# Kernel optimization log

Measured on AMD Instinct MI355X. Metric: run time of the kernel, lower is better.

Reference implementation:

```python
import jax, jax.numpy as jnp
import numpy as np

N, E, G = 100000, 600000, 64  # nodes, edges, graphs
F_IN, W, EPS = 32, 128, 1e-5


def setup_inputs() -> dict:
    key = jax.random.key(0)
    ks = jax.random.split(key, 16)
    p = lambda k, shape: jax.random.normal(k, shape, dtype=jnp.float32) * 0.1
    z = lambda n: jnp.zeros((n,), jnp.float32)
    o = lambda n: jnp.ones((n,), jnp.float32)
    return {
        "x": jax.random.normal(ks[0], (N, F_IN), dtype=jnp.float32),
        "edge_index": jax.random.randint(ks[1], (2, E), 0, N, dtype=jnp.int32),
        "batch": jnp.sort(jax.random.randint(ks[2], (N,), 0, G, dtype=jnp.int32)),
        # GCNConv layers
        "W1": p(ks[3], (F_IN, W)), "b1": z(W),
        "W2": p(ks[4], (W, W)), "b2": z(W),
        # mlp_first: Linear -> BN -> ReLU -> Linear
        "W3": p(ks[5], (W, W)), "b3": z(W), "g1": o(W), "be1": z(W),
        "W4": p(ks[6], (W, W)), "b4": z(W),
        # mlp: Linear -> BN -> ReLU -> Linear
        "W5": p(ks[7], (W, W // 2)), "b5": z(W // 2), "g2": o(W // 2), "be2": z(W // 2),
        "W6": p(ks[8], (W // 2, 1)), "b6": z(1),
    }


def gcn_conv(x, src, dst, Wt, b):
    # PyG GCNConv with add_self_loops=True: D^-1/2 (A+I) D^-1/2 (x W) + b
    h = x @ Wt  # [N, width]
    deg = jax.ops.segment_sum(jnp.ones(src.shape[0], x.dtype), dst, num_segments=N) + 1.0
    dinv = jax.lax.rsqrt(deg)
    norm = dinv[src] * dinv[dst]  # per-edge normalization
    agg = jax.ops.segment_sum(h[src] * norm[:, None], dst, num_segments=N)
    # self-loop term: norm for (i,i) is 1/deg[i]
    return agg + h * (dinv * dinv)[:, None] + b


def batch_norm(x, g, b):
    # training-mode BatchNorm1d (batch stats, biased var)
    mu = x.mean(axis=0)
    var = jnp.mean((x - mu) ** 2, axis=0)
    return (x - mu) * jax.lax.rsqrt(var + EPS) * g + b


def reference(x, edge_index, batch, W1, b1, W2, b2, W3, b3, g1, be1, W4, b4, W5, b5, g2, be2, W6, b6):
    src, dst = edge_index[0], edge_index[1]
    x = jax.nn.relu(gcn_conv(x, src, dst, W1, b1))
    x = jax.nn.relu(gcn_conv(x, src, dst, W2, b2))
    # mlp_first + ReLU
    x = jax.nn.relu(batch_norm(x @ W3 + b3, g1, be1)) @ W4 + b4
    x = jax.nn.relu(x)
    # global max pool over nodes per graph
    x = jax.ops.segment_max(x, batch, num_segments=G)  # [G, width]
    # final mlp
    x = jax.nn.relu(batch_norm(x @ W5 + b5, g2, be2)) @ W6 + b6
    return x[:, 0]
```

## Files before the change

kernel.cpp:

```cpp
#include <hip/hip_runtime.h>

#define N_NODES 100000
#define N_EDGES 600000
#define N_GRAPHS 64
#define EPS 1e-5f
#define SCAN_BLOCKS 391

typedef unsigned short u16;
typedef unsigned int u32;
typedef __attribute__((ext_vector_type(8))) short bf16x8;
typedef __attribute__((ext_vector_type(4))) float f32x4;

__device__ __forceinline__ float bf2f(u16 u) { return __uint_as_float(((u32)u) << 16); }
__device__ __forceinline__ u16 f2bf(float f) {
    u32 u = __float_as_uint(f);
    u += 0x7FFFu + ((u >> 16) & 1u);
    return (u16)(u >> 16);
}
__device__ __forceinline__ float2 bfx2(u32 v) {
    float2 r;
    r.x = __uint_as_float(v << 16);
    r.y = __uint_as_float(v & 0xFFFF0000u);
    return r;
}

#define WS_COUNTS   ((size_t)0)
#define WS_CURSOR   ((size_t)400384)
#define WS_POOLED   ((size_t)800768)
#define WS_BNSUM    ((size_t)833536)
#define WS_BNSUMSQ  ((size_t)834048)
#define WS_FLAG     ((size_t)834560)
#define ZERO_BYTES  ((size_t)835072)
#define WS_OFFSETS  ((size_t)835072)
#define WS_DINV     ((size_t)1235456)
#define WS_DINV2    ((size_t)1635840)
#define WS_SRCS     ((size_t)2036224)
#define WS_ZF       ((size_t)4436736)
#define WS_CANONW   ((size_t)4453120)
#define WS_BUFA     ((size_t)4578560)
#define WS_BUFB     ((size_t)30178560)

#define CW_W1 0
#define CW_B1 4096
#define CW_W2 4224
#define CW_B2 20608
#define CW_W3 20736
#define CW_B3 37120
#define CW_G1 37248
#define CW_BE1 37376
#define CW_W4 37504
#define CW_B4 53888
#define CW_W5 54016
#define CW_B5 62208
#define CW_G2 62272
#define CW_BE2 62336
#define CW_W6 62400
#define CW_B6 62464

__global__ void detect_kernel(const u32* __restrict__ xraw, int* __restrict__ flag) {
    __shared__ int cnt;
    if (threadIdx.x == 0) cnt = 0;
    __syncthreads();
    int c = 0;
    for (int i = threadIdx.x; i < 2048; i += 256) {
        u32 w = xraw[i];
        float a = fabsf(__uint_as_float((w & 0xFFFFu) << 16));
        if (a == 0.f || (a > 1e-8f && a < 1e4f)) c++;
    }
    atomicAdd(&cnt, c);
    __syncthreads();
    if (threadIdx.x == 0) *flag = (cnt > 1024) ? 1 : 0;
}

__global__ void convx_kernel(const void* __restrict__ xsrc, u16* __restrict__ dst,
                             const int* __restrict__ flag, const float* __restrict__ dinv) {
    int i = blockIdx.x * 256 + threadIdx.x;
    if (i < N_NODES * 32) {
        int r = i >> 5, c = i & 31;
        float v = (*flag) ? bf2f(((const u16*)xsrc)[i]) : ((const float*)xsrc)[i];
        dst[(size_t)(c >> 3) * (N_NODES * 8) + (size_t)r * 8 + (c & 7)] = f2bf(v * dinv[r]);
    }
}

struct SmallArgs {
    const void* src[16];
    int n[16];
    int off[16];
    int cols[16];
};
__global__ void convs_kernel(SmallArgs a, u16* __restrict__ dst, const int* __restrict__ flag) {
    int i = blockIdx.x * 256 + threadIdx.x;
    int isbf = *flag;
#pragma unroll
    for (int j = 0; j < 16; j++)
        if (i < a.n[j]) {
            u16 v = isbf ? ((const u16*)a.src[j])[i] : f2bf(((const float*)a.src[j])[i]);
            if (a.cols[j] > 0) {
                int k = i / a.cols[j];
                int n = i - k * a.cols[j];
                int Kd = a.n[j] / a.cols[j];
                dst[a.off[j] + n * Kd + k] = v;
            } else {
                dst[a.off[j] + i] = v;
            }
        }
}

__global__ void deg_kernel(const int* __restrict__ dst, int* __restrict__ counts) {
    int e = blockIdx.x * 256 + threadIdx.x;
    if (e < N_EDGES) atomicAdd(&counts[dst[e]], 1);
}

__global__ __launch_bounds__(256) void reduce_kernel(const int* __restrict__ counts,
                                                     int* __restrict__ partials) {
    int i = blockIdx.x * 256 + threadIdx.x;
    int v = (i < N_NODES) ? counts[i] : 0;
    for (int off = 32; off > 0; off >>= 1) v += __shfl_down(v, off, 64);
    __shared__ int wsum[4];
    if ((threadIdx.x & 63) == 0) wsum[threadIdx.x >> 6] = v;
    __syncthreads();
    if (threadIdx.x == 0) partials[blockIdx.x] = wsum[0] + wsum[1] + wsum[2] + wsum[3];
}

__global__ __launch_bounds__(512) void scanpart_kernel(int* __restrict__ partials) {
    __shared__ int sc[512];
    int t = threadIdx.x;
    int v = (t < SCAN_BLOCKS) ? partials[t] : 0;
    sc[t] = v;
    __syncthreads();
    for (int off = 1; off < 512; off <<= 1) {
        int u = (t >= off) ? sc[t - off] : 0;
        __syncthreads();
        sc[t] += u;
        __syncthreads();
    }
    if (t < SCAN_BLOCKS) partials[t] = sc[t] - v;
}

__global__ __launch_bounds__(256) void offsets_kernel(const int* __restrict__ counts,
                                                      const int* __restrict__ partials,
                                                      int* __restrict__ offs,
                                                      float* __restrict__ dinv) {
    int i = blockIdx.x * 256 + threadIdx.x;
    int lane = threadIdx.x & 63, wv = threadIdx.x >> 6;
    int v = (i < N_NODES) ? counts[i] : 0;
    int sv = v;
    for (int off = 1; off < 64; off <<= 1) {
        int u = __shfl_up(sv, off, 64);
        if (lane >= off) sv += u;
    }
    __shared__ int wsum[4];
    if (lane == 63) wsum[wv] = sv;
    __syncthreads();
    int wpre = 0;
    for (int w = 0; w < wv; w++) wpre += wsum[w];
    int excl = sv - v + wpre + partials[blockIdx.x];
    if (i < N_NODES) {
        offs[i] = excl;
        dinv[i] = rsqrtf((float)(v + 1));
    }
    if (i == N_NODES - 1) offs[N_NODES] = excl + v;
}

__global__ void scatter_kernel(const int* __restrict__ src, const int* __restrict__ dst,
                               const int* __restrict__ offs, int* __restrict__ cursor,
                               int* __restrict__ srcs) {
    int e = blockIdx.x * 256 + threadIdx.x;
    if (e < N_EDGES) {
        int d = dst[e];
        int p = offs[d] + atomicAdd(&cursor[d], 1);
        srcs[p] = src[e];
    }
}

__global__ __launch_bounds__(256, 8) void agg1_kernel(const u16* __restrict__ xs4,
                                                      const int* __restrict__ offs,
                                                      const int* __restrict__ srcs,
                                                      const float* __restrict__ dinv,
                                                      u16* __restrict__ axs) {
    const int p = blockIdx.x & 3;
    const int r = (blockIdx.x >> 2) * 256 + threadIdx.x;
    if (r >= N_NODES) return;
    const u16* base = xs4 + (size_t)p * (N_NODES * 8);
    float acc[8];
    {
        uint4 own = *(const uint4*)(base + (size_t)r * 8);
        u32 w4[4] = {own.x, own.y, own.z, own.w};
#pragma unroll
        for (int t = 0; t < 4; t++) {
            float2 f = bfx2(w4[t]);
            acc[2 * t] = f.x;
            acc[2 * t + 1] = f.y;
        }
    }
    const int e0 = offs[r], e1 = offs[r + 1];
    for (int e = e0; e < e1; e++) {
        int s = srcs[e];
        uint4 raw = *(const uint4*)(base + (size_t)s * 8);
        u32 w4[4] = {raw.x, raw.y, raw.z, raw.w};
#pragma unroll
        for (int t = 0; t < 4; t++) {
            float2 f = bfx2(w4[t]);
            acc[2 * t] += f.x;
            acc[2 * t + 1] += f.y;
        }
    }
    const float di = dinv[r];
    uint4 outv;
    u32* pk = (u32*)&outv;
#pragma unroll
    for (int t = 0; t < 4; t++)
        pk[t] = (u32)f2bf(acc[2 * t] * di) | ((u32)f2bf(acc[2 * t + 1] * di) << 16);
    *(uint4*)(axs + (size_t)r * 32 + p * 8) = outv;
}

__global__ __launch_bounds__(256, 8) void agg2_kernel(const u16* __restrict__ P2,
                                                      const int* __restrict__ offs,
                                                      const int* __restrict__ srcs,
                                                      const float* __restrict__ dinv,
                                                      const u16* __restrict__ b2,
                                                      u16* __restrict__ x2) {
    const int p = blockIdx.x & 7;
    const int t = threadIdx.x;
    const int r = (blockIdx.x >> 3) * 128 + (t >> 1);
    const int half = t & 1;
    if (r >= N_NODES) return;
    const u16* base = P2 + (size_t)p * (N_NODES * 16) + half * 8;
    float acc[8];
    {
        uint4 own = *(const uint4*)(base + (size_t)r * 16);
        u32 w4[4] = {own.x, own.y, own.z, own.w};
#pragma unroll
        for (int j = 0; j < 4; j++) {
            float2 f = bfx2(w4[j]);
            acc[2 * j] = f.x;
            acc[2 * j + 1] = f.y;
        }
    }
    const int e0 = offs[r], e1 = offs[r + 1];
    for (int e = e0; e < e1; e++) {
        int s = srcs[e];
        uint4 raw = *(const uint4*)(base + (size_t)s * 16);
        u32 w4[4] = {raw.x, raw.y, raw.z, raw.w};
#pragma unroll
        for (int j = 0; j < 4; j++) {
            float2 f = bfx2(w4[j]);
            acc[2 * j] += f.x;
            acc[2 * j + 1] += f.y;
        }
    }
    const float di = dinv[r];
    uint4 bb = *(const uint4*)(b2 + p * 16 + half * 8);
    u32 bw[4] = {bb.x, bb.y, bb.z, bb.w};
    uint4 outv;
    u32* pk = (u32*)&outv;
#pragma unroll
    for (int j = 0; j < 4; j++) {
        float2 fb = bfx2(bw[j]);
        float vx = fmaxf(fmaf(acc[2 * j], di, fb.x), 0.f);
        float vy = fmaxf(fmaf(acc[2 * j + 1], di, fb.y), 0.f);
        pk[j] = (u32)f2bf(vx) | ((u32)f2bf(vy) << 16);
    }
    *(uint4*)(x2 + (size_t)r * 128 + p * 16 + half * 8) = outv;
}

__global__ __launch_bounds__(256, 3) void gemmx_kernel(
    const u16* __restrict__ axs, const u16* __restrict__ W1t, const u16* __restrict__ b1,
    const u16* __restrict__ W2t, u16* __restrict__ P2, const float* __restrict__ dinv, int M) {
    __shared__ __align__(16) u16 ldsA[128 * 40];
    __shared__ __align__(16) u16 ldsB[128 * 136];

    const int tid = threadIdx.x;
    const int wave = tid >> 6;
    const int lane = tid & 63;
    const int l15 = lane & 15;
    const int quad = lane >> 4;
    const int row0 = blockIdx.x * 128 + wave * 32;

    {
        const u32* g = (const u32*)W1t;
        u32* l = (u32*)ldsA;
        for (int i = tid; i < 128 * 16; i += 256) {
            int n = i >> 4, j = i & 15;
            l[n * 20 + j] = g[i];
        }
    }
    {
        const u32* g = (const u32*)W2t;
        u32* l = (u32*)ldsB;
        for (int i = tid; i < 128 * 64; i += 256) {
            int n = i >> 6, j = i & 63;
            l[n * 68 + j] = g[i];
        }
    }

    uint4 gr1[2];
#pragma unroll
    for (int rt = 0; rt < 2; rt++) {
        int r = min(row0 + rt * 16 + l15, M - 1);
        gr1[rt] = *(const uint4*)(axs + (size_t)r * 32 + quad * 8);
    }
    __syncthreads();

    f32x4 acc1[2][8];
#pragma unroll
    for (int rt = 0; rt < 2; rt++)
#pragma unroll
        for (int nt = 0; nt < 8; nt++) acc1[rt][nt] = {0.f, 0.f, 0.f, 0.f};
#pragma unroll
    for (int nt = 0; nt < 8; nt++) {
        bf16x8 bf = *(const bf16x8*)&ldsA[(nt * 16 + l15) * 40 + quad * 8];
        acc1[0][nt] = __builtin_amdgcn_mfma_f32_16x16x32_bf16(
            __builtin_bit_cast(bf16x8, gr1[0]), bf, acc1[0][nt], 0, 0, 0);
        acc1[1][nt] = __builtin_amdgcn_mfma_f32_16x16x32_bf16(
            __builtin_bit_cast(bf16x8, gr1[1]), bf, acc1[1][nt], 0, 0, 0);
    }
    __syncthreads();

    float bcol[8];
#pragma unroll
    for (int nt = 0; nt < 8; nt++) bcol[nt] = bf2f(b1[nt * 16 + l15]);
    u16* tb = ldsA + wave * 1280;
    uint4 gr2[2][4];
#pragma unroll
    for (int kt = 0; kt < 4; kt++) {
#pragma unroll
        for (int rt = 0; rt < 2; rt++)
#pragma unroll
            for (int c2 = 0; c2 < 2; c2++) {
                int nt = 2 * kt + c2;
#pragma unroll
                for (int i = 0; i < 4; i++) {
                    float v = fmaxf(acc1[rt][nt][i] + bcol[nt], 0.f);
                    tb[(rt * 16 + quad * 4 + i) * 40 + c2 * 16 + l15] = f2bf(v);
                }
            }
#pragma unroll
        for (int rt = 0; rt < 2; rt++)
            gr2[rt][kt] = *(const uint4*)&tb[(rt * 16 + l15) * 40 + quad * 8];
    }

    f32x4 acc2[2][8];
#pragma unroll
    for (int rt = 0; rt < 2; rt++)
#pragma unroll
        for (int nt = 0; nt < 8; nt++) acc2[rt][nt] = {0.f, 0.f, 0.f, 0.f};
#pragma unroll
    for (int kt = 0; kt < 4; kt++) {
#pragma unroll
        for (int nt = 0; nt < 8; nt++) {
            bf16x8 bf = *(const bf16x8*)&ldsB[(nt * 16 + l15) * 136 + kt * 32 + quad * 8];
            acc2[0][nt] = __builtin_amdgcn_mfma_f32_16x16x32_bf16(
                __builtin_bit_cast(bf16x8, gr2[0][kt]), bf, acc2[0][nt], 0, 0, 0);
            acc2[1][nt] = __builtin_amdgcn_mfma_f32_16x16x32_bf16(
                __builtin_bit_cast(bf16x8, gr2[1][kt]), bf, acc2[1][nt], 0, 0, 0);
        }
    }

#pragma unroll
    for (int rt = 0; rt < 2; rt++)
#pragma unroll
        for (int i = 0; i < 4; i++) {
            int r = row0 + rt * 16 + quad * 4 + i;
            if (r < M) {
                float ds = dinv[r];
#pragma unroll
                for (int nt = 0; nt < 8; nt++)
                    P2[(size_t)nt * (N_NODES * 16) + (size_t)r * 16 + l15] =
                        f2bf(acc2[rt][nt][i] * ds);
            }
        }
}

__global__ __launch_bounds__(256, 3) void gemm3_kernel(
    const u16* __restrict__ A, const u16* __restrict__ Wt, const u16* __restrict__ bias,
    u16* __restrict__ C, float* __restrict__ bn_sum, float* __restrict__ bn_sumsq, int M) {
    constexpr int KP = 136;
    __shared__ __align__(16) u16 Wl[128 * KP];
    __shared__ float csum[128], csumsq[128];

    const int tid = threadIdx.x;
    const int wave = tid >> 6;
    const int lane = tid & 63;
    const int l15 = lane & 15;
    const int quad = lane >> 4;
    const int row0 = blockIdx.x * 128 + wave * 32;

    uint4 ra[2][4];
    int nd[2];
#pragma unroll
    for (int rt = 0; rt < 2; rt++) {
        nd[rt] = row0 + rt * 16 + l15;
        int r = min(nd[rt], M - 1);
        const u16* ap = A + (size_t)r * 128 + quad * 8;
#pragma unroll
        for (int kt = 0; kt < 4; kt++) ra[rt][kt] = *(const uint4*)(ap + kt * 32);
    }

    {
        const u32* g = (const u32*)Wt;
        u32* l = (u32*)Wl;
        for (int i = tid; i < 128 * 64; i += 256) {
            int n = i >> 6, j = i & 63;
            l[n * 68 + j] = g[i];
        }
    }
    if (tid < 128) {
        csum[tid] = 0.f;
        csumsq[tid] = 0.f;
    }
    __syncthreads();

    f32x4 acc[2][8];
#pragma unroll
    for (int rt = 0; rt < 2; rt++)
#pragma unroll
        for (int nt = 0; nt < 8; nt++) acc[rt][nt] = {0.f, 0.f, 0.f, 0.f};

#pragma unroll
    for (int kt = 0; kt < 4; kt++) {
        bf16x8 a0 = __builtin_bit_cast(bf16x8, ra[0][kt]);
        bf16x8 a1 = __builtin_bit_cast(bf16x8, ra[1][kt]);
#pragma unroll
        for (int nt = 0; nt < 8; nt++) {
            bf16x8 wf = *(const bf16x8*)&Wl[(nt * 16 + l15) * KP + kt * 32 + quad * 8];
            acc[0][nt] = __builtin_amdgcn_mfma_f32_16x16x32_bf16(wf, a0, acc[0][nt], 0, 0, 0);
            acc[1][nt] = __builtin_amdgcn_mfma_f32_16x16x32_bf16(wf, a1, acc[1][nt], 0, 0, 0);
        }
    }

    const bool ok0 = nd[0] < M, ok1 = nd[1] < M;
#pragma unroll
    for (int nt = 0; nt < 8; nt++) {
        uint2 braw = *(const uint2*)(bias + nt * 16 + quad * 4);
        float2 f0 = bfx2(braw.x), f1 = bfx2(braw.y);
        float bb[4] = {f0.x, f0.y, f1.x, f1.y};
        float v0[4], v1[4];
#pragma unroll
        for (int i = 0; i < 4; i++) {
            v0[i] = ok0 ? (acc[0][nt][i] + bb[i]) : 0.f;
            v1[i] = ok1 ? (acc[1][nt][i] + bb[i]) : 0.f;
        }
        if (ok0) {
            uint2 st;
            st.x = (u32)f2bf(v0[0]) | ((u32)f2bf(v0[1]) << 16);
            st.y = (u32)f2bf(v0[2]) | ((u32)f2bf(v0[3]) << 16);
            *(uint2*)(C + (size_t)nd[0] * 128 + nt * 16 + quad * 4) = st;
        }
        if (ok1) {
            uint2 st;
            st.x = (u32)f2bf(v1[0]) | ((u32)f2bf(v1[1]) << 16);
            st.y = (u32)f2bf(v1[2]) | ((u32)f2bf(v1[3]) << 16);
            *(uint2*)(C + (size_t)nd[1] * 128 + nt * 16 + quad * 4) = st;
        }
#pragma unroll
        for (int i = 0; i < 4; i++) {
            float s = v0[i] + v1[i];
            float q = v0[i] * v0[i] + v1[i] * v1[i];
#pragma unroll
            for (int m = 1; m < 16; m <<= 1) {
                s += __shfl_xor(s, m);
                q += __shfl_xor(q, m);
            }
            if (l15 == 0) {
                atomicAdd(&csum[nt * 16 + quad * 4 + i], s);
                atomicAdd(&csumsq[nt * 16 + quad * 4 + i], q);
            }
        }
    }
    __syncthreads();
    if (tid < 128) {
        atomicAdd(&bn_sum[tid], csum[tid]);
        atomicAdd(&bn_sumsq[tid], csumsq[tid]);
    }
}

__global__ __launch_bounds__(256, 3) void gemm4_kernel(
    const u16* __restrict__ A, const u16* __restrict__ Wt, const u16* __restrict__ bias,
    const float* __restrict__ scl, const float* __restrict__ shf,
    const int* __restrict__ batch, u32* __restrict__ pooled, int M) {
    constexpr int KP = 136;
    __shared__ __align__(16) u16 Wl[128 * KP];
    __shared__ u32 lmax[4 * 128];

    const int tid = threadIdx.x;
    const int wave = tid >> 6;
    const int lane = tid & 63;
    const int l15 = lane & 15;
    const int quad = lane >> 4;
    const int row0 = blockIdx.x * 128 + wave * 32;

    uint4 ra[2][4];
#pragma unroll
    for (int rt = 0; rt < 2; rt++) {
        int r = min(row0 + rt * 16 + l15, M - 1);
        const u16* ap = A + (size_t)r * 128 + quad * 8;
#pragma unroll
        for (int kt = 0; kt < 4; kt++) ra[rt][kt] = *(const uint4*)(ap + kt * 32);
    }

    {
        const u32* g = (const u32*)Wt;
        u32* l = (u32*)Wl;
        for (int i = tid; i < 128 * 64; i += 256) {
            int n = i >> 6, j = i & 63;
            l[n * 68 + j] = g[i];
        }
    }
    for (int i = tid; i < 512; i += 256) lmax[i] = 0u;

    const int base = blockIdx.x * 128;
    const int gfirst = batch[min(base, M - 1)];
    const int glast = batch[min(base + 127, M - 1)];
    const bool fast = (glast - gfirst) < 4;
    __syncthreads();

    f32x4 acc[2][8];
#pragma unroll
    for (int rt = 0; rt < 2; rt++)
#pragma unroll
        for (int nt = 0; nt < 8; nt++) acc[rt][nt] = {0.f, 0.f, 0.f, 0.f};

#pragma unroll
    for (int kt = 0; kt < 4; kt++) {
        float s8[8], h8[8];
#pragma unroll
        for (int t = 0; t < 8; t++) {
            s8[t] = scl[kt * 32 + quad * 8 + t];
            h8[t] = shf[kt * 32 + quad * 8 + t];
        }
        bf16x8 af[2];
#pragma unroll
        for (int rt = 0; rt < 2; rt++) {
            u32 w4[4] = {ra[rt][kt].x, ra[rt][kt].y, ra[rt][kt].z, ra[rt][kt].w};
            bf16x8 tmp;
#pragma unroll
            for (int t = 0; t < 4; t++) {
                float2 f = bfx2(w4[t]);
                f.x = fmaxf(fmaf(f.x, s8[2 * t], h8[2 * t]), 0.f);
                f.y = fmaxf(fmaf(f.y, s8[2 * t + 1], h8[2 * t + 1]), 0.f);
                tmp[2 * t] = (short)f2bf(f.x);
                tmp[2 * t + 1] = (short)f2bf(f.y);
            }
            af[rt] = tmp;
        }
#pragma unroll
        for (int nt = 0; nt < 8; nt++) {
            bf16x8 bf = *(const bf16x8*)&Wl[(nt * 16 + l15) * KP + kt * 32 + quad * 8];
            acc[0][nt] = __builtin_amdgcn_mfma_f32_16x16x32_bf16(af[0], bf, acc[0][nt], 0, 0, 0);
            acc[1][nt] = __builtin_amdgcn_mfma_f32_16x16x32_bf16(af[1], bf, acc[1][nt], 0, 0, 0);
        }
    }

    float b[8];
#pragma unroll
    for (int nt = 0; nt < 8; nt++) b[nt] = bf2f(bias[nt * 16 + l15]);
    float cur[8];
#pragma unroll
    for (int nt = 0; nt < 8; nt++) cur[nt] = 0.f;
    int curg = -1;
#pragma unroll
    for (int rt = 0; rt < 2; rt++)
#pragma unroll
        for (int i = 0; i < 4; i++) {
            int r = row0 + rt * 16 + quad * 4 + i;
            if (r < M) {
                int g = batch[r];
                if (g != curg) {
                    if (curg >= 0) {
#pragma unroll
                        for (int nt = 0; nt < 8; nt++)
                            if (cur[nt] > 0.f) {
                                u32 bits = __float_as_uint(cur[nt]);
                                if (fast)
                                    atomicMax(&lmax[(curg - gfirst) * 128 + nt * 16 + l15], bits);
                                else
                                    atomicMax(&pooled[curg * 128 + nt * 16 + l15], bits);
                            }
                    }
                    curg = g;
#pragma unroll
                    for (int nt = 0; nt < 8; nt++) cur[nt] = 0.f;
                }
#pragma unroll
                for (int nt = 0; nt < 8; nt++)
                    cur[nt] = fmaxf(cur[nt], fmaxf(acc[rt][nt][i] + b[nt], 0.f));
            }
        }
    if (curg >= 0) {
#pragma unroll
        for (int nt = 0; nt < 8; nt++)
            if (cur[nt] > 0.f) {
                u32 bits = __float_as_uint(cur[nt]);
                if (fast)
                    atomicMax(&lmax[(curg - gfirst) * 128 + nt * 16 + l15], bits);
                else
                    atomicMax(&pooled[curg * 128 + nt * 16 + l15], bits);
            }
    }
    __syncthreads();
    if (fast) {
        int ngr = glast - gfirst + 1;
        for (int i = tid; i < ngr * 128; i += 256) {
            u32 v = lmax[i];
            if (v) atomicMax(&pooled[gfirst * 128 + i], v);
        }
    }
}

__global__ void bnstats_kernel(float* __restrict__ bn_sum, float* __restrict__ bn_sumsq,
                               const u16* __restrict__ g1, const u16* __restrict__ be1) {
    int c = threadIdx.x;
    if (c < 128) {
        float mu = bn_sum[c] / (float)N_NODES;
        float var = bn_sumsq[c] / (float)N_NODES - mu * mu;
        float rstd = rsqrtf(var + EPS);
        float sc = rstd * bf2f(g1[c]);
        bn_sum[c] = sc;
        bn_sumsq[c] = bf2f(be1[c]) - mu * sc;
    }
}

__global__ __launch_bounds__(256) void head1_kernel(const u32* __restrict__ pooled,
                                                    const u16* __restrict__ W5,
                                                    const u16* __restrict__ b5,
                                                    float* __restrict__ zf) {
    __shared__ float red[4][64];
    int g = blockIdx.x;
    int c = threadIdx.x & 63;
    int kq = threadIdx.x >> 6;
    const u32* prow = pooled + g * 128;
    float p = 0.f;
    for (int k = kq * 32; k < kq * 32 + 32; k++)
        p = fmaf(__uint_as_float(prow[k]), bf2f(W5[k * 64 + c]), p);
    red[kq][c] = p;
    __syncthreads();
    if (kq == 0) zf[g * 64 + c] = red[0][c] + red[1][c] + red[2][c] + red[3][c] + bf2f(b5[c]);
}

__global__ __launch_bounds__(64) void head2_kernel(const float* __restrict__ zf,
                                                   const u16* __restrict__ g2,
                                                   const u16* __restrict__ be2,
                                                   const u16* __restrict__ W6,
                                                   const u16* __restrict__ b6,
                                                   void* __restrict__ outv,
                                                   const int* __restrict__ flag) {
    __shared__ float Z[64][65];
    __shared__ float sc[64], sh[64], w6[64];
    int t = threadIdx.x;
    for (int idx = t; idx < 4096; idx += 64) Z[idx >> 6][idx & 63] = zf[idx];
    w6[t] = bf2f(W6[t]);
    __syncthreads();
    {
        float s = 0.f, sq = 0.f;
        for (int g = 0; g < 64; g++) {
            float v = Z[g][t];
            s += v;
            sq += v * v;
        }
        float mu = s * (1.f / 64.f);
        float var = sq * (1.f / 64.f) - mu * mu;
        float rstd = rsqrtf(var + EPS);
        float scale = rstd * bf2f(g2[t]);
        sc[t] = scale;
        sh[t] = bf2f(be2[t]) - mu * scale;
    }
    __syncthreads();
    float o = 0.f;
    for (int c = 0; c < 64; c++)
        o = fmaf(fmaxf(fmaf(Z[t][c], sc[c], sh[c]), 0.f), w6[c], o);
    float res = o + bf2f(b6[0]);
    if (*flag)
        ((u16*)outv)[t] = f2bf(res);
    else
        ((float*)outv)[t] = res;
}

extern "C" void kernel_launch(void* const* d_in, const int* in_sizes, int n_in, void* d_out,
                              int out_size, void* d_ws, size_t ws_size, hipStream_t stream) {
    const void* x = d_in[0];
    const int* ei = (const int*)d_in[1];
    const int* bat = (const int*)d_in[2];

    char* ws = (char*)d_ws;
    int* counts = (int*)(ws + WS_COUNTS);
    int* cursor = (int*)(ws + WS_CURSOR);
    u32* pooled = (u32*)(ws + WS_POOLED);
    float* bnsum = (float*)(ws + WS_BNSUM);
    float* bnssq = (float*)(ws + WS_BNSUMSQ);
    int* flag = (int*)(ws + WS_FLAG);
    int* offs = (int*)(ws + WS_OFFSETS);
    float* dinv = (float*)(ws + WS_DINV);
    int* partials = (int*)(ws + WS_DINV2);
    int* srcs = (int*)(ws + WS_SRCS);
    float* zf = (float*)(ws + WS_ZF);
    u16* cw = (u16*)(ws + WS_CANONW);
    u16* P2 = (u16*)(ws + WS_BUFA);
    u16* xs4 = (u16*)(ws + WS_BUFB);
    u16* axs = (u16*)(ws + WS_BUFB) + 3200000;
    u16* x2 = (u16*)(ws + WS_BUFB);

    const int* esrc = ei;
    const int* edst = ei + N_EDGES;

    hipMemsetAsync(ws, 0, ZERO_BYTES, stream);
    detect_kernel<<<1, 256, 0, stream>>>((const u32*)x, flag);

    SmallArgs sa;
    const int cw_off[16] = {CW_W1, CW_B1, CW_W2, CW_B2, CW_W3, CW_B3, CW_G1, CW_BE1,
                            CW_W4, CW_B4, CW_W5, CW_B5, CW_G2, CW_BE2, CW_W6, CW_B6};
    const int cw_n[16] = {4096, 128, 16384, 128, 16384, 128, 128, 128,
                          16384, 128, 8192, 64, 64, 64, 64, 1};
    const int cw_c[16] = {128, 0, 128, 0, 128, 0, 0, 0, 128, 0, 0, 0, 0, 0, 0, 0};
    for (int j = 0; j < 16; j++) {
        sa.src[j] = d_in[3 + j];
        sa.n[j] = cw_n[j];
        sa.off[j] = cw_off[j];
        sa.cols[j] = cw_c[j];
    }
    convs_kernel<<<64, 256, 0, stream>>>(sa, cw, flag);

    deg_kernel<<<(N_EDGES + 255) / 256, 256, 0, stream>>>(edst, counts);
    reduce_kernel<<<SCAN_BLOCKS, 256, 0, stream>>>(counts, partials);
    scanpart_kernel<<<1, 512, 0, stream>>>(partials);
    offsets_kernel<<<SCAN_BLOCKS, 256, 0, stream>>>(counts, partials, offs, dinv);
    scatter_kernel<<<(N_EDGES + 255) / 256, 256, 0, stream>>>(esrc, edst, offs, cursor, srcs);
    convx_kernel<<<(N_NODES * 32 + 255) / 256, 256, 0, stream>>>(x, xs4, flag, dinv);

    const int gb = (N_NODES + 127) / 128;
    agg1_kernel<<<4 * SCAN_BLOCKS, 256, 0, stream>>>(xs4, offs, srcs, dinv, axs);
    gemmx_kernel<<<gb, 256, 0, stream>>>(axs, cw + CW_W1, cw + CW_B1, cw + CW_W2, P2, dinv,
                                         N_NODES);
    agg2_kernel<<<8 * gb, 256, 0, stream>>>(P2, offs, srcs, dinv, cw + CW_B2, x2);
    gemm3_kernel<<<gb, 256, 0, stream>>>(x2, cw + CW_W3, cw + CW_B3, x2, bnsum, bnssq, N_NODES);
    bnstats_kernel<<<1, 128, 0, stream>>>(bnsum, bnssq, cw + CW_G1, cw + CW_BE1);
    gemm4_kernel<<<gb, 256, 0, stream>>>(x2, cw + CW_W4, cw + CW_B4, bnsum, bnssq, bat, pooled,
                                         N_NODES);
    head1_kernel<<<N_GRAPHS, 256, 0, stream>>>(pooled, cw + CW_W5, cw + CW_B5, zf);
    head2_kernel<<<1, 64, 0, stream>>>(zf, cw + CW_G2, cw + CW_BE2, cw + CW_W6, cw + CW_B6,
                                       d_out, flag);
}
```

Measured before the change: 333.6 us.

## Unroll gather loops by four and store x2 in feature-plane layout

The edge-gather loops in agg1 and agg2 now load four neighbour indices and rows at a time, using clamped indices and zero masks for the tail, so more memory loads are in flight per thread. Launch bounds drop from 8 to 4 waves per SIMD to give the unroll more registers. agg2 output, gemm3 input/output and gemm4 input move from row-major 128-wide rows to eight 16-feature planes. The plane layout keeps each agg2 block's writes contiguous, but the GEMMs now read A with strided plane accesses and may waste a little bandwidth on masked tail loads.

```diff
diff --git a/kernel.cpp b/kernel.cpp
--- a/kernel.cpp
+++ b/kernel.cpp
@@ -173,7 +173,7 @@
     }
 }
 
-__global__ __launch_bounds__(256, 8) void agg1_kernel(const u16* __restrict__ xs4,
+__global__ __launch_bounds__(256, 4) void agg1_kernel(const u16* __restrict__ xs4,
                                                       const int* __restrict__ offs,
                                                       const int* __restrict__ srcs,
                                                       const float* __restrict__ dinv,
@@ -194,15 +194,28 @@
         }
     }
     const int e0 = offs[r], e1 = offs[r + 1];
-    for (int e = e0; e < e1; e++) {
-        int s = srcs[e];
-        uint4 raw = *(const uint4*)(base + (size_t)s * 8);
-        u32 w4[4] = {raw.x, raw.y, raw.z, raw.w};
-#pragma unroll
-        for (int t = 0; t < 4; t++) {
-            float2 f = bfx2(w4[t]);
-            acc[2 * t] += f.x;
-            acc[2 * t + 1] += f.y;
+    for (int e = e0; e < e1; e += 4) {
+        int ss[4];
+        float mm[4];
+        ss[0] = srcs[e];
+        mm[0] = 1.f;
+#pragma unroll
+        for (int j = 1; j < 4; j++) {
+            ss[j] = srcs[min(e + j, e1 - 1)];
+            mm[j] = (e + j < e1) ? 1.f : 0.f;
+        }
+        uint4 rr[4];
+#pragma unroll
+        for (int j = 0; j < 4; j++) rr[j] = *(const uint4*)(base + (size_t)ss[j] * 8);
+#pragma unroll
+        for (int j = 0; j < 4; j++) {
+            u32 w4[4] = {rr[j].x, rr[j].y, rr[j].z, rr[j].w};
+#pragma unroll
+            for (int t = 0; t < 4; t++) {
+                float2 f = bfx2(w4[t]);
+                acc[2 * t] = fmaf(f.x, mm[j], acc[2 * t]);
+                acc[2 * t + 1] = fmaf(f.y, mm[j], acc[2 * t + 1]);
+            }
         }
     }
     const float di = dinv[r];
@@ -214,12 +227,12 @@
     *(uint4*)(axs + (size_t)r * 32 + p * 8) = outv;
 }
 
-__global__ __launch_bounds__(256, 8) void agg2_kernel(const u16* __restrict__ P2,
+__global__ __launch_bounds__(256, 4) void agg2_kernel(const u16* __restrict__ P2,
                                                       const int* __restrict__ offs,
                                                       const int* __restrict__ srcs,
                                                       const float* __restrict__ dinv,
                                                       const u16* __restrict__ b2,
-                                                      u16* __restrict__ x2) {
+                                                      u16* __restrict__ x2p) {
     const int p = blockIdx.x & 7;
     const int t = threadIdx.x;
     const int r = (blockIdx.x >> 3) * 128 + (t >> 1);
@@ -238,15 +251,28 @@
         }
     }
     const int e0 = offs[r], e1 = offs[r + 1];
-    for (int e = e0; e < e1; e++) {
-        int s = srcs[e];
-        uint4 raw = *(const uint4*)(base + (size_t)s * 16);
-        u32 w4[4] = {raw.x, raw.y, raw.z, raw.w};
+    for (int e = e0; e < e1; e += 4) {
+        int ss[4];
+        float mm[4];
+        ss[0] = srcs[e];
+        mm[0] = 1.f;
+#pragma unroll
+        for (int j = 1; j < 4; j++) {
+            ss[j] = srcs[min(e + j, e1 - 1)];
+            mm[j] = (e + j < e1) ? 1.f : 0.f;
+        }
+        uint4 rr[4];
+#pragma unroll
+        for (int j = 0; j < 4; j++) rr[j] = *(const uint4*)(base + (size_t)ss[j] * 16);
 #pragma unroll
         for (int j = 0; j < 4; j++) {
-            float2 f = bfx2(w4[j]);
-            acc[2 * j] += f.x;
-            acc[2 * j + 1] += f.y;
+            u32 w4[4] = {rr[j].x, rr[j].y, rr[j].z, rr[j].w};
+#pragma unroll
+            for (int k = 0; k < 4; k++) {
+                float2 f = bfx2(w4[k]);
+                acc[2 * k] = fmaf(f.x, mm[j], acc[2 * k]);
+                acc[2 * k + 1] = fmaf(f.y, mm[j], acc[2 * k + 1]);
+            }
         }
     }
     const float di = dinv[r];
@@ -261,7 +287,7 @@
         float vy = fmaxf(fmaf(acc[2 * j + 1], di, fb.y), 0.f);
         pk[j] = (u32)f2bf(vx) | ((u32)f2bf(vy) << 16);
     }
-    *(uint4*)(x2 + (size_t)r * 128 + p * 16 + half * 8) = outv;
+    *(uint4*)(x2p + (size_t)p * (N_NODES * 16) + (size_t)r * 16 + half * 8) = outv;
 }
 
 __global__ __launch_bounds__(256, 3) void gemmx_kernel(
@@ -392,9 +418,12 @@
     for (int rt = 0; rt < 2; rt++) {
         nd[rt] = row0 + rt * 16 + l15;
         int r = min(nd[rt], M - 1);
-        const u16* ap = A + (size_t)r * 128 + quad * 8;
-#pragma unroll
-        for (int kt = 0; kt < 4; kt++) ra[rt][kt] = *(const uint4*)(ap + kt * 32);
+#pragma unroll
+        for (int kt = 0; kt < 4; kt++) {
+            int plane = 2 * kt + (quad >> 1);
+            ra[rt][kt] = *(const uint4*)(A + (size_t)plane * (N_NODES * 16) + (size_t)r * 16 +
+                                         (quad & 1) * 8);
+        }
     }
 
     {
@@ -441,17 +470,18 @@
             v0[i] = ok0 ? (acc[0][nt][i] + bb[i]) : 0.f;
             v1[i] = ok1 ? (acc[1][nt][i] + bb[i]) : 0.f;
         }
+        u16* Cp = C + (size_t)nt * (N_NODES * 16);
         if (ok0) {
             uint2 st;
             st.x = (u32)f2bf(v0[0]) | ((u32)f2bf(v0[1]) << 16);
             st.y = (u32)f2bf(v0[2]) | ((u32)f2bf(v0[3]) << 16);
-            *(uint2*)(C + (size_t)nd[0] * 128 + nt * 16 + quad * 4) = st;
+            *(uint2*)(Cp + (size_t)nd[0] * 16 + quad * 4) = st;
         }
         if (ok1) {
             uint2 st;
             st.x = (u32)f2bf(v1[0]) | ((u32)f2bf(v1[1]) << 16);
             st.y = (u32)f2bf(v1[2]) | ((u32)f2bf(v1[3]) << 16);
-            *(uint2*)(C + (size_t)nd[1] * 128 + nt * 16 + quad * 4) = st;
+            *(uint2*)(Cp + (size_t)nd[1] * 16 + quad * 4) = st;
         }
 #pragma unroll
         for (int i = 0; i < 4; i++) {
@@ -494,9 +524,12 @@
 #pragma unroll
     for (int rt = 0; rt < 2; rt++) {
         int r = min(row0 + rt * 16 + l15, M - 1);
-        const u16* ap = A + (size_t)r * 128 + quad * 8;
-#pragma unroll
-        for (int kt = 0; kt < 4; kt++) ra[rt][kt] = *(const uint4*)(ap + kt * 32);
+#pragma unroll
+        for (int kt = 0; kt < 4; kt++) {
+            int plane = 2 * kt + (quad >> 1);
+            ra[rt][kt] = *(const uint4*)(A + (size_t)plane * (N_NODES * 16) + (size_t)r * 16 +
+                                         (quad & 1) * 8);
+        }
     }
 
     {
@@ -698,7 +731,7 @@
     u16* P2 = (u16*)(ws + WS_BUFA);
     u16* xs4 = (u16*)(ws + WS_BUFB);
     u16* axs = (u16*)(ws + WS_BUFB) + 3200000;
-    u16* x2 = (u16*)(ws + WS_BUFB);
+    u16* x2p = (u16*)(ws + WS_BUFB);
 
     const int* esrc = ei;
     const int* edst = ei + N_EDGES;
@@ -731,10 +764,11 @@
     agg1_kernel<<<4 * SCAN_BLOCKS, 256, 0, stream>>>(xs4, offs, srcs, dinv, axs);
     gemmx_kernel<<<gb, 256, 0, stream>>>(axs, cw + CW_W1, cw + CW_B1, cw + CW_W2, P2, dinv,
                                          N_NODES);
-    agg2_kernel<<<8 * gb, 256, 0, stream>>>(P2, offs, srcs, dinv, cw + CW_B2, x2);
-    gemm3_kernel<<<gb, 256, 0, stream>>>(x2, cw + CW_W3, cw + CW_B3, x2, bnsum, bnssq, N_NODES);
+    agg2_kernel<<<8 * gb, 256, 0, stream>>>(P2, offs, srcs, dinv, cw + CW_B2, x2p);
+    gemm3_kernel<<<gb, 256, 0, stream>>>(x2p, cw + CW_W3, cw + CW_B3, x2p, bnsum, bnssq,
+                                         N_NODES);
     bnstats_kernel<<<1, 128, 0, stream>>>(bnsum, bnssq, cw + CW_G1, cw + CW_BE1);
-    gemm4_kernel<<<gb, 256, 0, stream>>>(x2, cw + CW_W4, cw + CW_B4, bnsum, bnssq, bat, pooled,
+    gemm4_kernel<<<gb, 256, 0, stream>>>(x2p, cw + CW_W4, cw + CW_B4, bnsum, bnssq, bat, pooled,
                                          N_NODES);
     head1_kernel<<<N_GRAPHS, 256, 0, stream>>>(pooled, cw + CW_W5, cw + CW_B5, zf);
     head2_kernel<<<1, 64, 0, stream>>>(zf, cw + CW_G2, cw + CW_BE2, cw + CW_W6, cw + CW_B6,
```

Measured after the change: 316.7 us. 1.05x faster.
